# Performance work log

Hardware: AMD Instinct MI355X
Metric: run time of the kernel (lower is better)

Reference implementation:

```python
import jax, jax.numpy as jnp
import numpy as np

N = 4096  # number of nodes (matches fill_max of edge indices)


def _dense(edges, n):
    # edges: [2, E] int; dense {0,1} adjacency. Duplicate edges collapse (set semantics).
    return jnp.zeros((n, n), dtype=jnp.float32).at[edges[0], edges[1]].set(1.0)


def setup_inputs() -> dict:
    key = jax.random.key(0)
    ks = jax.random.split(key, 4)
    E = 200000
    mk = lambda k: jax.random.randint(k, (2, E), 0, N, dtype=jnp.int32)
    return {
        "A_pos_t": mk(ks[0]),
        "A_pos_tp1": mk(ks[1]),
        "A_neg_t": mk(ks[2]),
        "A_neg_tp1": mk(ks[3]),
    }


def reference(A_pos_t, A_pos_tp1, A_neg_t, A_neg_tp1):
    p_t = _dense(A_pos_t, N)
    p1 = _dense(A_pos_tp1, N)
    n_t = _dense(A_neg_t, N)
    n1 = _dense(A_neg_tp1, N)

    # edge_index_diff: set symmetric difference == elementwise xor of {0,1} adjacency
    xor_p = p_t + p1 - 2.0 * p_t * p1
    xor_n = n_t + n1 - 2.0 * n_t * n1

    # Balance theory triangle closure on (tp1) graphs.
    # sign(a,b): +1 if pos edge (pos checked first -> priority), -1 elif neg edge.
    sp = p1                      # positive-sign edge indicator
    sn = n1 * (1.0 - p1)         # negative-sign edge indicator (pos has priority)
    off = 1.0 - jnp.eye(N, dtype=jnp.float32)
    spo = sp * off               # exclude b==a / b==c (triples are distinct)
    sno = sn * off

    # number of 2-paths a->b->c with predicted sign +1 / -1
    M_same = spo @ spo + sno @ sno
    M_diff = spo @ sno + sno @ spo

    # the Python loop only infers edges (a,c) with a < c (orientations (i,j,k),(i,k,j),(j,i,k))
    tri = jnp.triu(jnp.ones((N, N), dtype=jnp.float32), k=1)

    ind_p = M_same * tri * (1.0 - p1)  # skip pairs already positively connected
    ind_n = M_diff * tri * (1.0 - n1)  # skip pairs already negatively connected

    # Output: [2, N, N]; entry = xor indicator + indirect-edge multiplicity count
    return jnp.stack([xor_p + ind_p, xor_n + ind_n])
```

## Files before the change

### kernel.cpp

```cpp
#include <hip/hip_runtime.h>


#define NN 4096
#define NW 128
#define MASK_BYTES ((size_t)NN * NW * 4)
#define MASK_WORDS ((size_t)NN * NW)

typedef unsigned int u32;
typedef __attribute__((ext_vector_type(4))) int int4v;
typedef __attribute__((ext_vector_type(4))) float f32x4;

__device__ __forceinline__ void gload_lds16(const char* g, char* l) {
    __builtin_amdgcn_global_load_lds(
        (const __attribute__((address_space(1))) void*)g,
        (__attribute__((address_space(3))) void*)l, 16, 0, 0);
}


__global__ void zero_ws(int4v* __restrict__ p) {
    p[blockIdx.x * 256 + threadIdx.x] = int4v{0, 0, 0, 0};
}

__global__ void scatter_all(const int* __restrict__ e0, const int* __restrict__ e1,
                            const int* __restrict__ e2, const int* __restrict__ e3,
                            int E0, int E1, int E2, int E3,
                            u32* __restrict__ ws) {
    int i = blockIdx.x * blockDim.x + threadIdx.x;
    u32* Pt = ws + 0 * MASK_WORDS;
    u32* P1 = ws + 1 * MASK_WORDS;
    u32* Nt = ws + 2 * MASK_WORDS;
    u32* N1 = ws + 3 * MASK_WORDS;
    if (i < E0) { int r = e0[i], c = e0[i + E0];
        atomicOr(&Pt[r * NW + (c >> 5)], 1u << (c & 31)); }
    if (i < E1) { int r = e1[i], c = e1[i + E1];
        atomicOr(&P1[r * NW + (c >> 5)], 1u << (c & 31)); }
    if (i < E2) { int r = e2[i], c = e2[i + E2];
        atomicOr(&Nt[r * NW + (c >> 5)], 1u << (c & 31)); }
    if (i < E3) { int r = e3[i], c = e3[i + E3];
        atomicOr(&N1[r * NW + (c >> 5)], 1u << (c & 31)); }
}

__device__ __forceinline__ int4v expand_e(u32 sp, u32 sn) {
    int4v E;
    #pragma unroll
    for (int i = 0; i < 4; i++) {
        u32 p = (((sp >> (4 * i)) & 0xFu) * 0x00204081u) & 0x01010101u;
        u32 n = (((sn >> (4 * i)) & 0xFu) * 0x00204081u) & 0x01010101u;
        E[i] = (int)(p | (n << 5));
    }
    return E;
}

__global__ void build_both(const u32* __restrict__ masks,
                           char* __restrict__ E, char* __restrict__ ET) {
    const u32* P  = masks + 1 * MASK_WORDS;
    const u32* Nm = masks + 3 * MASK_WORDS;
    if (blockIdx.x < 2048) {
        int w = blockIdx.x * 256 + threadIdx.x;
        u32 p = P[w];
        u32 n = Nm[w] & ~p;
        int a = w >> 7, col = w & 127;
        if ((a >> 5) == col) {
            u32 db = 1u << (a & 31);
            p &= ~db; n &= ~db;
        }
        char* dst = E + (size_t)a * NN + col * 32;
        *reinterpret_cast<int4v*>(dst)      = expand_e(p & 0xFFFFu, n & 0xFFFFu);
        *reinterpret_cast<int4v*>(dst + 16) = expand_e(p >> 16, n >> 16);
    } else {
        int gw = (blockIdx.x - 2048) * 4 + (threadIdx.x >> 6);
        int lane = threadIdx.x & 63;
        int ab = gw >> 7;
        int wc = gw & 127;
        u32 pw = P[(ab * 64 + lane) * NW + wc];
        u32 nw = Nm[(ab * 64 + lane) * NW + wc];
        u32 myp = 0, myn = 0;
        #pragma unroll
        for (int j = 0; j < 32; j++) {
            unsigned long long bp = __ballot((pw >> j) & 1u);
            unsigned long long bn = __ballot((nw >> j) & 1u);
            if ((lane & 31) == j) {
                myp = (lane < 32) ? (u32)bp : (u32)(bp >> 32);
                myn = (lane < 32) ? (u32)bn : (u32)(bn >> 32);
            }
        }
        u32 p = myp;
        u32 n = myn & ~p;
        int c = wc * 32 + (lane & 31);
        int abase = ab * 64 + (lane >> 5) * 32;
        if (c >= abase && c < abase + 32) {
            u32 db = 1u << (c - abase);
            p &= ~db; n &= ~db;
        }
        char* dst = ET + (size_t)c * NN + abase;
        *reinterpret_cast<int4v*>(dst)      = expand_e(p & 0xFFFFu, n & 0xFFFFu);
        *reinterpret_cast<int4v*>(dst + 16) = expand_e(p >> 16, n >> 16);
    }
}

__global__ __launch_bounds__(512, 4) void gemm_ep(
    const char* __restrict__ E, const char* __restrict__ ET,
    const u32* __restrict__ Pt, const u32* __restrict__ P1,
    const u32* __restrict__ Nt, const u32* __restrict__ N1,
    float* __restrict__ out)
{
    const int tid = threadIdx.x;
    const size_t plane = (size_t)NN * NN;

    int s_ = ((int)blockIdx.x & 7) * 66 + ((int)blockIdx.x >> 3);
    int by = (int)((65.0f - sqrtf(4225.0f - 8.0f * (float)s_)) * 0.5f);
    if (by > 31) by = 31;
    while (by > 0 && 32 * by - (by * (by - 1)) / 2 > s_) --by;
    while (32 * (by + 1) - ((by + 1) * by) / 2 <= s_) ++by;
    int bx = by + s_ - (32 * by - (by * (by - 1)) / 2);
    const int a0 = by << 7, c0 = bx << 7;

    __shared__ char LB[2][2][16384];

    const int wave = tid >> 6, lane = tid & 63;
    const int wr = (wave >> 1) * 32, wcol = (wave & 1) * 64;
    const int lr = lane & 15, lg = lane >> 4;

    const int srow = tid >> 3;
    const int sslot = tid & 7;
    const int soff = ((sslot ^ (srow & 7)) << 4);
    const char* gA0 = E  + (size_t)(a0 + srow)      * NN + soff;
    const char* gA1 = E  + (size_t)(a0 + 64 + srow) * NN + soff;
    const char* gB0 = ET + (size_t)(c0 + srow)      * NN + soff;
    const char* gB1 = ET + (size_t)(c0 + 64 + srow) * NN + soff;
    const int t16 = tid * 16;

    int4v acc[2][4];
    int4v zero = {0, 0, 0, 0};
    #pragma unroll
    for (int m = 0; m < 2; m++)
        #pragma unroll
        for (int n = 0; n < 4; n++) acc[m][n] = zero;

    #define STAGE(b, p)                                           \
        do {                                                      \
            const int koff = (p) * 128;                           \
            gload_lds16(gA0 + koff, &LB[b][0][t16]);              \
            gload_lds16(gA1 + koff, &LB[b][0][8192 + t16]);       \
            gload_lds16(gB0 + koff, &LB[b][1][t16]);              \
            gload_lds16(gB1 + koff, &LB[b][1][8192 + t16]);       \
        } while (0)

    #define COMPUTE(b)                                                          \
        do {                                                                    \
            _Pragma("unroll")                                                   \
            for (int ks = 0; ks < 2; ks++) {                                    \
                int4v bf[4];                                                    \
                _Pragma("unroll")                                               \
                for (int n = 0; n < 4; n++) {                                   \
                    int rowb = wcol + n * 16 + lr;                              \
                    bf[n] = *reinterpret_cast<const int4v*>(&LB[b][1][          \
                        rowb * 128 + (((ks * 4 + lg) ^ (rowb & 7)) << 4)]);     \
                }                                                               \
                __builtin_amdgcn_s_setprio(1);                                  \
                _Pragma("unroll")                                               \
                for (int m = 0; m < 2; m++) {                                   \
                    int rowa = wr + m * 16 + lr;                                \
                    int4v af = *reinterpret_cast<const int4v*>(&LB[b][0][       \
                        rowa * 128 + (((ks * 4 + lg) ^ (rowa & 7)) << 4)]);     \
                    _Pragma("unroll")                                           \
                    for (int n = 0; n < 4; n++)                                 \
                        acc[m][n] = __builtin_amdgcn_mfma_i32_16x16x64_i8(      \
                            af, bf[n], acc[m][n], 0, 0, 0);                     \
                }                                                               \
                __builtin_amdgcn_s_setprio(0);                                  \
            }                                                                   \
        } while (0)

    STAGE(0, 0);
    asm volatile("s_waitcnt vmcnt(0)" ::: "memory");
    __builtin_amdgcn_s_barrier();

    int cur = 0;
    for (int p = 0; p < 31; ++p) {
        STAGE(cur ^ 1, p + 1);
        COMPUTE(cur);
        asm volatile("s_waitcnt vmcnt(0)" ::: "memory");
        __builtin_amdgcn_s_barrier();
        cur ^= 1;
    }
    COMPUTE(cur);
    #undef STAGE
    #undef COMPUTE

    #pragma unroll
    for (int m = 0; m < 2; m++) {
        #pragma unroll
        for (int n = 0; n < 4; n++) {
            #pragma unroll
            for (int q = 0; q < 4; q++) {
                int a = a0 + wr + m * 16 + lg * 4 + q;
                int c = c0 + wcol + n * 16 + lr;
                int widx = a * NW + (c >> 5);
                int bit = c & 31;
                u32 p1 = (P1[widx] >> bit) & 1u;
                u32 n1 = (N1[widx] >> bit) & 1u;
                u32 pt = (Pt[widx] >> bit) & 1u;
                u32 nt = (Nt[widx] >> bit) & 1u;
                int av = acc[m][n][q];
                int Ms = (av & 31) + (av >> 10);
                int Md = (av >> 5) & 31;
                int o0 = (int)(pt ^ p1) + ((a < c && !p1) ? Ms : 0);
                int o1 = (int)(nt ^ n1) + ((a < c && !n1) ? Md : 0);
                size_t oi = (size_t)a * NN + c;
                out[oi] = (float)o0;
                out[plane + oi] = (float)o1;
            }
        }
    }

    if (by != bx) {
        #pragma unroll 4
        for (int pass = 0; pass < 8; ++pass) {
            int e = pass * 2048 + tid * 4;
            int r = e >> 7, cc = e & 127;
            int widx = (c0 + r) * NW + ((a0 + cc) >> 5);
            int sh = cc & 31;
            u32 xp = (P1[widx] ^ Pt[widx]) >> sh;
            u32 xn = (N1[widx] ^ Nt[widx]) >> sh;
            f32x4 o0, o1;
            #pragma unroll
            for (int i = 0; i < 4; i++) {
                o0[i] = (float)((xp >> i) & 1u);
                o1[i] = (float)((xn >> i) & 1u);
            }
            size_t ob = (size_t)(c0 + r) * NN + a0 + cc;
            *reinterpret_cast<f32x4*>(out + ob) = o0;
            *reinterpret_cast<f32x4*>(out + plane + ob) = o1;
        }
    }
}

extern "C" void kernel_launch(void* const* d_in, const int* in_sizes, int n_in,
                              void* d_out, int out_size, void* d_ws, size_t ws_size,
                              hipStream_t stream) {
    char* ws = (char*)d_ws;
    u32* masks = (u32*)ws;
    u32* Pt = masks + 0 * MASK_WORDS;
    u32* P1 = masks + 1 * MASK_WORDS;
    u32* Nt = masks + 2 * MASK_WORDS;
    u32* N1 = masks + 3 * MASK_WORDS;
    char* E  = ws + 4 * MASK_BYTES;
    char* ET = E + (size_t)NN * NN;

    zero_ws<<<2048, 256, 0, stream>>>((int4v*)masks);

    int E0 = in_sizes[0] / 2, E1 = in_sizes[1] / 2;
    int E2 = in_sizes[2] / 2, E3 = in_sizes[3] / 2;
    int Emax = max(max(E0, E1), max(E2, E3));
    scatter_all<<<(Emax + 255) / 256, 256, 0, stream>>>(
        (const int*)d_in[0], (const int*)d_in[1], (const int*)d_in[2],
        (const int*)d_in[3], E0, E1, E2, E3, masks);

    build_both<<<4096, 256, 0, stream>>>(masks, E, ET);

    gemm_ep<<<528, 512, 0, stream>>>(E, ET, Pt, P1, Nt, N1, (float*)d_out);
}
```

Baseline: 128.2 us.

## Use 256x256 GEMM tiles and dedicate separate blocks to lower-triangle xor writes

Enlarges the upper-triangular GEMM tile from 128x128 to 256x256, with each wave computing a 128x64 sub-tile, which raises data reuse per LDS load. The lower-triangle xor-only output is moved out of the GEMM blocks into dedicated blocks (ids 136-255), giving 256 blocks in total. The cost is much higher register and LDS use (acc[8][4] and 128KB of LDS), so occupancy drops to one block per CU. Fewer blocks than CUs may also leave some compute units idle, and the GEMM and xor-only blocks carry unequal amounts of work.

```diff
diff --git a/kernel.cpp b/kernel.cpp
--- a/kernel.cpp
+++ b/kernel.cpp
@@ -98,7 +98,7 @@
     }
 }
 
-__global__ __launch_bounds__(512, 4) void gemm_ep(
+__global__ __launch_bounds__(512, 1) void gemm_ep(
     const char* __restrict__ E, const char* __restrict__ ET,
     const u32* __restrict__ Pt, const u32* __restrict__ P1,
     const u32* __restrict__ Nt, const u32* __restrict__ N1,
@@ -107,43 +107,69 @@
     const int tid = threadIdx.x;
     const size_t plane = (size_t)NN * NN;
 
-    int s_ = ((int)blockIdx.x & 7) * 66 + ((int)blockIdx.x >> 3);
-    int by = (int)((65.0f - sqrtf(4225.0f - 8.0f * (float)s_)) * 0.5f);
-    if (by > 31) by = 31;
-    while (by > 0 && 32 * by - (by * (by - 1)) / 2 > s_) --by;
-    while (32 * (by + 1) - ((by + 1) * by) / 2 <= s_) ++by;
-    int bx = by + s_ - (32 * by - (by * (by - 1)) / 2);
-    const int a0 = by << 7, c0 = bx << 7;
-
-    __shared__ char LB[2][2][16384];
+    const int id = ((int)blockIdx.x & 7) * 32 + ((int)blockIdx.x >> 3);
+
+    if (id >= 136) {
+        int j = id - 136;
+        int R = 1;
+        while ((R + 1) * R / 2 <= j) ++R;
+        int C = j - R * (R - 1) / 2;
+        const int r0 = R << 8, c0l = C << 8;
+        #pragma unroll 4
+        for (int pass = 0; pass < 32; ++pass) {
+            int e = pass * 2048 + tid * 4;
+            int r = e >> 8, cc = e & 255;
+            int widx = (r0 + r) * NW + ((c0l + cc) >> 5);
+            int sh = cc & 31;
+            u32 xp = (P1[widx] ^ Pt[widx]) >> sh;
+            u32 xn = (N1[widx] ^ Nt[widx]) >> sh;
+            f32x4 o0, o1;
+            #pragma unroll
+            for (int i = 0; i < 4; i++) {
+                o0[i] = (float)((xp >> i) & 1u);
+                o1[i] = (float)((xn >> i) & 1u);
+            }
+            size_t ob = (size_t)(r0 + r) * NN + c0l + cc;
+            *reinterpret_cast<f32x4*>(out + ob) = o0;
+            *reinterpret_cast<f32x4*>(out + plane + ob) = o1;
+        }
+        return;
+    }
+
+    int by = 0;
+    while (16 * (by + 1) - ((by + 1) * by) / 2 <= id) ++by;
+    int bx = by + id - (16 * by - (by * (by - 1)) / 2);
+    const int a0 = by << 8, c0 = bx << 8;
+
+    __shared__ char LB[2][2][32768];
 
     const int wave = tid >> 6, lane = tid & 63;
-    const int wr = (wave >> 1) * 32, wcol = (wave & 1) * 64;
+    const int wr = (wave >> 2) * 128;
+    const int wcol = (wave & 3) * 64;
     const int lr = lane & 15, lg = lane >> 4;
 
-    const int srow = tid >> 3;
-    const int sslot = tid & 7;
-    const int soff = ((sslot ^ (srow & 7)) << 4);
-    const char* gA0 = E  + (size_t)(a0 + srow)      * NN + soff;
-    const char* gA1 = E  + (size_t)(a0 + 64 + srow) * NN + soff;
-    const char* gB0 = ET + (size_t)(c0 + srow)      * NN + soff;
-    const char* gB1 = ET + (size_t)(c0 + 64 + srow) * NN + soff;
+    const int soff = (((tid & 7) ^ ((tid >> 3) & 7)) << 4);
+    const char* gA = E  + (size_t)(a0 + (tid >> 3)) * NN + soff;
+    const char* gB = ET + (size_t)(c0 + (tid >> 3)) * NN + soff;
     const int t16 = tid * 16;
 
-    int4v acc[2][4];
+    int4v acc[8][4];
     int4v zero = {0, 0, 0, 0};
     #pragma unroll
-    for (int m = 0; m < 2; m++)
+    for (int m = 0; m < 8; m++)
         #pragma unroll
         for (int n = 0; n < 4; n++) acc[m][n] = zero;
 
-    #define STAGE(b, p)                                           \
-        do {                                                      \
-            const int koff = (p) * 128;                           \
-            gload_lds16(gA0 + koff, &LB[b][0][t16]);              \
-            gload_lds16(gA1 + koff, &LB[b][0][8192 + t16]);       \
-            gload_lds16(gB0 + koff, &LB[b][1][t16]);              \
-            gload_lds16(gB1 + koff, &LB[b][1][8192 + t16]);       \
+    #define STAGE(b, p)                                                     \
+        do {                                                                \
+            const size_t koff = (size_t)(p) * 128;                          \
+            _Pragma("unroll")                                               \
+            for (int g = 0; g < 4; g++) {                                   \
+                gload_lds16(gA + (size_t)g * 64 * NN + koff,                \
+                            &LB[b][0][g * 8192 + t16]);                     \
+                gload_lds16(gB + (size_t)g * 64 * NN + koff,                \
+                            &LB[b][1][g * 8192 + t16]);                     \
+            }                                                               \
         } while (0)
 
     #define COMPUTE(b)                                                          \
@@ -159,7 +185,7 @@
                 }                                                               \
                 __builtin_amdgcn_s_setprio(1);                                  \
                 _Pragma("unroll")                                               \
-                for (int m = 0; m < 2; m++) {                                   \
+                for (int m = 0; m < 8; m++) {                                   \
                     int rowa = wr + m * 16 + lr;                                \
                     int4v af = *reinterpret_cast<const int4v*>(&LB[b][0][       \
                         rowa * 128 + (((ks * 4 + lg) ^ (rowa & 7)) << 4)]);     \
@@ -189,7 +215,7 @@
     #undef COMPUTE
 
     #pragma unroll
-    for (int m = 0; m < 2; m++) {
+    for (int m = 0; m < 8; m++) {
         #pragma unroll
         for (int n = 0; n < 4; n++) {
             #pragma unroll
@@ -213,27 +239,6 @@
             }
         }
     }
-
-    if (by != bx) {
-        #pragma unroll 4
-        for (int pass = 0; pass < 8; ++pass) {
-            int e = pass * 2048 + tid * 4;
-            int r = e >> 7, cc = e & 127;
-            int widx = (c0 + r) * NW + ((a0 + cc) >> 5);
-            int sh = cc & 31;
-            u32 xp = (P1[widx] ^ Pt[widx]) >> sh;
-            u32 xn = (N1[widx] ^ Nt[widx]) >> sh;
-            f32x4 o0, o1;
-            #pragma unroll
-            for (int i = 0; i < 4; i++) {
-                o0[i] = (float)((xp >> i) & 1u);
-                o1[i] = (float)((xn >> i) & 1u);
-            }
-            size_t ob = (size_t)(c0 + r) * NN + a0 + cc;
-            *reinterpret_cast<f32x4*>(out + ob) = o0;
-            *reinterpret_cast<f32x4*>(out + plane + ob) = o1;
-        }
-    }
 }
 
 extern "C" void kernel_launch(void* const* d_in, const int* in_sizes, int n_in,
@@ -259,5 +264,5 @@
 
     build_both<<<4096, 256, 0, stream>>>(masks, E, ET);
 
-    gemm_ep<<<528, 512, 0, stream>>>(E, ET, Pt, P1, Nt, N1, (float*)d_out);
-}
+    gemm_ep<<<256, 512, 0, stream>>>(E, ET, Pt, P1, Nt, N1, (float*)d_out);
+}
```

Result: slower. 133.2 us (+3.9%).
